# Optimization experiments

Measured on AMD Instinct MI355X. Metric: run time of the kernel, lower is better.

The kernel has to match this reference:

```python
import jax, jax.numpy as jnp
import numpy as np

N_NODES = 50000
N_EDGES = 800000
IN_CH = 128
OUT_CH = 32
HID = 2 * OUT_CH  # 64


def gcn_layer(x, W, b, src, dst, n):
    """PyG GCNConv: x' = D^-1/2 (A + I) D^-1/2 (x W) + b, flow source->target."""
    h = x @ W  # [n, out]
    # degree on target nodes, +1 for self loop
    deg = jax.ops.segment_sum(jnp.ones(dst.shape[0], h.dtype), dst, num_segments=n) + 1.0
    dis = jax.lax.rsqrt(deg)  # deg^-1/2
    norm = dis[src] * dis[dst]  # [E]
    msg = h[src] * norm[:, None]  # gather + scale, [E, out]
    agg = jax.ops.segment_sum(msg, dst, num_segments=n)  # scatter-add
    # self-loop contribution has norm dis[i]*dis[i] = 1/deg[i]
    return agg + h * (dis * dis)[:, None] + b


def setup_inputs() -> dict:
    key = jax.random.key(0)
    k1, k2, k3, k4, k5, k6 = jax.random.split(key, 6)
    x = jax.random.normal(k1, (N_NODES, IN_CH), dtype=jnp.float32)
    edge_index = jax.random.randint(k2, (2, N_EDGES), 0, N_NODES, dtype=jnp.int64)
    # Glorot-style init for GCN weights
    W1 = jax.random.normal(k3, (IN_CH, HID), dtype=jnp.float32) / np.sqrt(IN_CH)
    b1 = jnp.zeros((HID,), dtype=jnp.float32)
    W2 = jax.random.normal(k4, (HID, OUT_CH), dtype=jnp.float32) / np.sqrt(HID)
    b2 = jnp.zeros((OUT_CH,), dtype=jnp.float32)
    return {"x": x, "W1": W1, "b1": b1, "W2": W2, "b2": b2, "edge_index": edge_index}


def reference(x, W1, b1, W2, b2, edge_index):
    src, dst = edge_index[0], edge_index[1]
    h = jax.nn.relu(gcn_layer(x, W1, b1, src, dst, N_NODES))
    out = gcn_layer(h, W2, b2, src, dst, N_NODES)
    return out
```

## Files before the change

kernel.cpp:

```cpp
#include <hip/hip_runtime.h>
#include <hip/hip_bf16.h>
#include <cstddef>
#include <cstdint>

#define N_NODES 50000
#define N_EDGES 800000
#define IN_CH 128
#define HID 64
#define OUT_CH 32

#define NBUCK 196
#define BCAP2 5120
#define NBLK 256
#define EPB 3125
#define NT1 782

typedef __attribute__((ext_vector_type(8))) short bf16x8;
typedef __attribute__((ext_vector_type(8))) unsigned short u16x8;
typedef __attribute__((ext_vector_type(4))) float f32x4;

__device__ __forceinline__ unsigned short bf16rne(float f) {
    union { float f; unsigned u; } c; c.f = f;
    unsigned r = c.u + 0x7FFF + ((c.u >> 16) & 1);
    return (unsigned short)(r >> 16);
}
__device__ __forceinline__ float bf16f(unsigned short b) {
    union { unsigned u; float f; } c; c.u = ((unsigned)b) << 16;
    return c.f;
}

__device__ __forceinline__ void load_edge(const void* ei, int flag, int e, int& s, int& d) {
    if (flag) {
        const long long* p = (const long long*)ei;
        s = (int)p[e];
        d = (int)p[e + N_EDGES];
    } else {
        const int* p = (const int*)ei;
        s = p[e];
        d = p[e + N_EDGES];
    }
}

__global__ __launch_bounds__(256) void zerocur_kernel(int* __restrict__ cursor) {
    if (threadIdx.x < NBUCK) cursor[threadIdx.x] = 0;
}

__global__ __launch_bounds__(256) void scatter1_kernel(const void* ei,
                                                       int* __restrict__ cursor,
                                                       unsigned* __restrict__ packed) {
    __shared__ unsigned cbuf[EPB];
    __shared__ int h[NBUCK];
    __shared__ int lcur[NBUCK];
    __shared__ unsigned red[256];
    const int t = threadIdx.x;
    const int base = blockIdx.x * EPB;

    {
        unsigned acc = 0;
        const unsigned* w = (const unsigned*)ei;
        for (int i = t; i < 2048; i += 256) acc |= w[2 * i + 1];
        red[t] = acc;
    }
    if (t < NBUCK) h[t] = 0;
    __syncthreads();
    if (t < 128) red[t] |= red[t + 128];
    __syncthreads();
    if (t < 64) red[t] |= red[t + 64];
    __syncthreads();
    if (t == 0) {
        unsigned q = 0;
        for (int i = 0; i < 64; ++i) q |= red[i];
        red[0] = q;
    }
    __syncthreads();
    const int flag = (red[0] == 0) ? 1 : 0;

    for (int i = t; i < EPB; i += 256) {
        int s, d;
        load_edge(ei, flag, base + i, s, d);
        cbuf[i] = (unsigned)s | ((unsigned)d << 16);
        atomicAdd(&h[d >> 8], 1);
    }
    __syncthreads();
    if (t < NBUCK) lcur[t] = h[t] ? (t * BCAP2 + atomicAdd(&cursor[t], h[t])) : 0;
    __syncthreads();
    for (int i = t; i < EPB; i += 256) {
        unsigned p = cbuf[i];
        int b = p >> 24;
        int pos = atomicAdd(&lcur[b], 1);
        packed[pos] = p;
    }
}

__global__ __launch_bounds__(256) void buckgemm1_kernel(
        const int* __restrict__ cursor, unsigned* __restrict__ packed,
        unsigned* __restrict__ rowinfo, float* __restrict__ dis,
        const float* __restrict__ x, const float* __restrict__ W1,
        unsigned short* __restrict__ h1b) {
    __shared__ union {
        struct { int cnt[256]; int pref[256]; int lbuf[BCAP2]; } bk;
        struct { unsigned short xa[64][136]; unsigned short wb[64][136]; } g1;
    } u;
    const int t = threadIdx.x;

    if (blockIdx.x < NBUCK) {
        const int b = blockIdx.x;
        const int nodebase = b << 8;
        const int rbase = b * BCAP2;
        const int bsize = cursor[b];
        const int nb = min(256, N_NODES - nodebase);

        u.bk.cnt[t] = 0;
        __syncthreads();
        for (int i = t; i < bsize; i += 256)
            atomicAdd(&u.bk.cnt[(packed[rbase + i] >> 16) & 255], 1);
        __syncthreads();
        const int deg = u.bk.cnt[t];
        u.bk.pref[t] = deg;
        __syncthreads();
        for (int off = 1; off < 256; off <<= 1) {
            int q = (t >= off) ? u.bk.pref[t - off] : 0;
            __syncthreads();
            u.bk.pref[t] += q;
            __syncthreads();
        }
        const int excl = u.bk.pref[t] - deg;
        if (t < nb) {
            rowinfo[nodebase + t] = (unsigned)(rbase + excl) | ((unsigned)deg << 20);
            dis[nodebase + t] = rsqrtf((float)deg + 1.0f);
        }
        __syncthreads();
        u.bk.cnt[t] = excl;
        __syncthreads();
        for (int i = t; i < bsize; i += 256) {
            unsigned p = packed[rbase + i];
            int pos = atomicAdd(&u.bk.cnt[(p >> 16) & 255], 1);
            u.bk.lbuf[pos] = (int)(p & 0xFFFFu);
        }
        __syncthreads();
        for (int i = t; i < bsize; i += 256)
            packed[rbase + i] = (unsigned)u.bk.lbuf[i];
    } else {
        const int w = t >> 6;
        const int l = t & 63;
        const int brow = (blockIdx.x - NBUCK) * 64;

        for (int f = t; f < 64 * 32; f += 256) {
            int r = f >> 5, c = (f & 31) << 2;
            int gr = brow + r;
            float4 v = (gr < N_NODES) ? *(const float4*)(x + gr * IN_CH + c)
                                      : make_float4(0.f, 0.f, 0.f, 0.f);
            u.g1.xa[r][c + 0] = bf16rne(v.x); u.g1.xa[r][c + 1] = bf16rne(v.y);
            u.g1.xa[r][c + 2] = bf16rne(v.z); u.g1.xa[r][c + 3] = bf16rne(v.w);
        }
        for (int f = t; f < 128 * 16; f += 256) {
            int k = f >> 4, n = (f & 15) << 2;
            float4 v = *(const float4*)(W1 + k * HID + n);
            u.g1.wb[n + 0][k] = bf16rne(v.x); u.g1.wb[n + 1][k] = bf16rne(v.y);
            u.g1.wb[n + 2][k] = bf16rne(v.z); u.g1.wb[n + 3][k] = bf16rne(v.w);
        }
        __syncthreads();

        const int fr = l & 15;
        const int fk = (l >> 4) << 3;
        f32x4 acc[4] = {{0.f,0.f,0.f,0.f},{0.f,0.f,0.f,0.f},
                        {0.f,0.f,0.f,0.f},{0.f,0.f,0.f,0.f}};
#pragma unroll
        for (int kb = 0; kb < 4; ++kb) {
            const int k = kb * 32 + fk;
            bf16x8 a = *(const bf16x8*)&u.g1.xa[w * 16 + fr][k];
#pragma unroll
            for (int n = 0; n < 4; ++n) {
                bf16x8 bfr = *(const bf16x8*)&u.g1.wb[n * 16 + fr][k];
                acc[n] = __builtin_amdgcn_mfma_f32_16x16x32_bf16(a, bfr, acc[n], 0, 0, 0);
            }
        }
        const int rb = brow + w * 16 + ((l >> 4) << 2);
#pragma unroll
        for (int n = 0; n < 4; ++n) {
#pragma unroll
            for (int i = 0; i < 4; ++i) {
                int r = rb + i;
                if (r < N_NODES) h1b[r * HID + n * 16 + fr] = bf16rne(acc[n][i]);
            }
        }
    }
}

__global__ __launch_bounds__(256) void agg1_kernel(
        const unsigned* __restrict__ rowinfo, const unsigned* __restrict__ sorted,
        const float* __restrict__ dis, const unsigned short* __restrict__ h1b,
        const float* __restrict__ b1, unsigned short* __restrict__ agg1b) {
    const int l = threadIdx.x & 63;
    const int g = l >> 3;
    const int cl = l & 7;
    const int d = blockIdx.x * 4 + (threadIdx.x >> 6);
    if (d >= N_NODES) return;
    const unsigned ri = rowinfo[d];
    const int beg = (int)(ri & 0xFFFFFu);
    const int end = beg + (int)(ri >> 20);
    const float dd = dis[d];
    float a0 = 0.f, a1 = 0.f, a2 = 0.f, a3 = 0.f;
    float a4 = 0.f, a5 = 0.f, a6 = 0.f, a7 = 0.f;
    for (int j = beg + g; j < end; j += 8) {
        int s = (int)sorted[j];
        float n = dis[s] * dd;
        bf16x8 h = *(const bf16x8*)(h1b + s * HID + 8 * cl);
        a0 += bf16f((unsigned short)h[0]) * n; a1 += bf16f((unsigned short)h[1]) * n;
        a2 += bf16f((unsigned short)h[2]) * n; a3 += bf16f((unsigned short)h[3]) * n;
        a4 += bf16f((unsigned short)h[4]) * n; a5 += bf16f((unsigned short)h[5]) * n;
        a6 += bf16f((unsigned short)h[6]) * n; a7 += bf16f((unsigned short)h[7]) * n;
    }
#pragma unroll
    for (int st = 8; st <= 32; st <<= 1) {
        a0 += __shfl_xor(a0, st, 64); a1 += __shfl_xor(a1, st, 64);
        a2 += __shfl_xor(a2, st, 64); a3 += __shfl_xor(a3, st, 64);
        a4 += __shfl_xor(a4, st, 64); a5 += __shfl_xor(a5, st, 64);
        a6 += __shfl_xor(a6, st, 64); a7 += __shfl_xor(a7, st, 64);
    }
    if (g == 0) {
        bf16x8 hs = *(const bf16x8*)(h1b + d * HID + 8 * cl);
        float4 bv0 = *(const float4*)(b1 + 8 * cl);
        float4 bv1 = *(const float4*)(b1 + 8 * cl + 4);
        float d2 = dd * dd;
        u16x8 o;
        o[0] = bf16rne(fmaxf(a0 + bf16f((unsigned short)hs[0]) * d2 + bv0.x, 0.f));
        o[1] = bf16rne(fmaxf(a1 + bf16f((unsigned short)hs[1]) * d2 + bv0.y, 0.f));
        o[2] = bf16rne(fmaxf(a2 + bf16f((unsigned short)hs[2]) * d2 + bv0.z, 0.f));
        o[3] = bf16rne(fmaxf(a3 + bf16f((unsigned short)hs[3]) * d2 + bv0.w, 0.f));
        o[4] = bf16rne(fmaxf(a4 + bf16f((unsigned short)hs[4]) * d2 + bv1.x, 0.f));
        o[5] = bf16rne(fmaxf(a5 + bf16f((unsigned short)hs[5]) * d2 + bv1.y, 0.f));
        o[6] = bf16rne(fmaxf(a6 + bf16f((unsigned short)hs[6]) * d2 + bv1.z, 0.f));
        o[7] = bf16rne(fmaxf(a7 + bf16f((unsigned short)hs[7]) * d2 + bv1.w, 0.f));
        *(u16x8*)(agg1b + d * HID + 8 * cl) = o;
    }
}

__global__ __launch_bounds__(256) void gemm2_kernel(
        const unsigned short* __restrict__ agg1b, const float* __restrict__ W2,
        unsigned short* __restrict__ h2b) {
    __shared__ unsigned short xa[64][72];
    __shared__ unsigned short wb[32][72];
    const int t = threadIdx.x;
    const int w = t >> 6;
    const int l = t & 63;
    const int brow = blockIdx.x * 64;

    for (int f = t; f < 64 * 16; f += 256) {
        int r = f >> 4, c = (f & 15) << 2;
        int gr = brow + r;
        ushort4 v = make_ushort4(0, 0, 0, 0);
        if (gr < N_NODES) v = *(const ushort4*)(agg1b + gr * HID + c);
        *(ushort4*)&xa[r][c] = v;
    }
    for (int f = t; f < 64 * 8; f += 256) {
        int k = f >> 3, n = (f & 7) << 2;
        float4 v = *(const float4*)(W2 + k * OUT_CH + n);
        wb[n + 0][k] = bf16rne(v.x); wb[n + 1][k] = bf16rne(v.y);
        wb[n + 2][k] = bf16rne(v.z); wb[n + 3][k] = bf16rne(v.w);
    }
    __syncthreads();

    const int fr = l & 15;
    const int fk = (l >> 4) << 3;
    f32x4 acc[2] = {{0.f,0.f,0.f,0.f},{0.f,0.f,0.f,0.f}};
#pragma unroll
    for (int kb = 0; kb < 2; ++kb) {
        const int k = kb * 32 + fk;
        bf16x8 a = *(const bf16x8*)&xa[w * 16 + fr][k];
#pragma unroll
        for (int n = 0; n < 2; ++n) {
            bf16x8 bfr = *(const bf16x8*)&wb[n * 16 + fr][k];
            acc[n] = __builtin_amdgcn_mfma_f32_16x16x32_bf16(a, bfr, acc[n], 0, 0, 0);
        }
    }
    const int rb = brow + w * 16 + ((l >> 4) << 2);
#pragma unroll
    for (int n = 0; n < 2; ++n) {
#pragma unroll
        for (int i = 0; i < 4; ++i) {
            int r = rb + i;
            if (r < N_NODES) h2b[r * OUT_CH + n * 16 + fr] = bf16rne(acc[n][i]);
        }
    }
}

__global__ __launch_bounds__(256) void agg2_kernel(
        const unsigned* __restrict__ rowinfo, const unsigned* __restrict__ sorted,
        const float* __restrict__ dis, const unsigned short* __restrict__ h2b,
        const float* __restrict__ b2, float* __restrict__ out) {
    const int l = threadIdx.x & 63;
    const int g = l >> 2;
    const int cl = l & 3;
    const int d = blockIdx.x * 4 + (threadIdx.x >> 6);
    if (d >= N_NODES) return;
    const unsigned ri = rowinfo[d];
    const int beg = (int)(ri & 0xFFFFFu);
    const int end = beg + (int)(ri >> 20);
    const float dd = dis[d];
    float a0 = 0.f, a1 = 0.f, a2 = 0.f, a3 = 0.f;
    float a4 = 0.f, a5 = 0.f, a6 = 0.f, a7 = 0.f;
    for (int j = beg + g; j < end; j += 16) {
        int s = (int)sorted[j];
        float n = dis[s] * dd;
        bf16x8 h = *(const bf16x8*)(h2b + s * OUT_CH + 8 * cl);
        a0 += bf16f((unsigned short)h[0]) * n; a1 += bf16f((unsigned short)h[1]) * n;
        a2 += bf16f((unsigned short)h[2]) * n; a3 += bf16f((unsigned short)h[3]) * n;
        a4 += bf16f((unsigned short)h[4]) * n; a5 += bf16f((unsigned short)h[5]) * n;
        a6 += bf16f((unsigned short)h[6]) * n; a7 += bf16f((unsigned short)h[7]) * n;
    }
#pragma unroll
    for (int st = 4; st <= 32; st <<= 1) {
        a0 += __shfl_xor(a0, st, 64); a1 += __shfl_xor(a1, st, 64);
        a2 += __shfl_xor(a2, st, 64); a3 += __shfl_xor(a3, st, 64);
        a4 += __shfl_xor(a4, st, 64); a5 += __shfl_xor(a5, st, 64);
        a6 += __shfl_xor(a6, st, 64); a7 += __shfl_xor(a7, st, 64);
    }
    if (g == 0) {
        bf16x8 hs = *(const bf16x8*)(h2b + d * OUT_CH + 8 * cl);
        float4 bv0 = *(const float4*)(b2 + 8 * cl);
        float4 bv1 = *(const float4*)(b2 + 8 * cl + 4);
        float d2 = dd * dd;
        float4 o0, o1;
        o0.x = a0 + bf16f((unsigned short)hs[0]) * d2 + bv0.x;
        o0.y = a1 + bf16f((unsigned short)hs[1]) * d2 + bv0.y;
        o0.z = a2 + bf16f((unsigned short)hs[2]) * d2 + bv0.z;
        o0.w = a3 + bf16f((unsigned short)hs[3]) * d2 + bv0.w;
        o1.x = a4 + bf16f((unsigned short)hs[4]) * d2 + bv1.x;
        o1.y = a5 + bf16f((unsigned short)hs[5]) * d2 + bv1.y;
        o1.z = a6 + bf16f((unsigned short)hs[6]) * d2 + bv1.z;
        o1.w = a7 + bf16f((unsigned short)hs[7]) * d2 + bv1.w;
        *(float4*)(out + d * OUT_CH + 8 * cl) = o0;
        *(float4*)(out + d * OUT_CH + 8 * cl + 4) = o1;
    }
}

extern "C" void kernel_launch(void* const* d_in, const int* in_sizes, int n_in,
                              void* d_out, int out_size, void* d_ws, size_t ws_size,
                              hipStream_t stream) {
    const float* x  = (const float*)d_in[0];
    const float* W1 = (const float*)d_in[1];
    const float* b1 = (const float*)d_in[2];
    const float* W2 = (const float*)d_in[3];
    const float* b2 = (const float*)d_in[4];
    const void*  ei = d_in[5];
    float* out = (float*)d_out;

    char* wp = (char*)d_ws;
    auto alloc = [&](size_t n) { char* p = wp; wp += (n + 511) & ~(size_t)511; return p; };
    int*   cursor  = (int*)alloc(NBUCK * 4);
    unsigned* rowinfo = (unsigned*)alloc((size_t)N_NODES * 4);
    float* dis     = (float*)alloc((size_t)N_NODES * 4);
    unsigned* packed = (unsigned*)alloc((size_t)NBUCK * BCAP2 * 4);
    unsigned short* h1b = (unsigned short*)alloc((size_t)N_NODES * HID * 2);
    unsigned short* agg1b = (unsigned short*)alloc((size_t)N_NODES * HID * 2);
    unsigned short* h2b = (unsigned short*)alloc((size_t)N_NODES * OUT_CH * 2);

    zerocur_kernel<<<1, 256, 0, stream>>>(cursor);
    scatter1_kernel<<<NBLK, 256, 0, stream>>>(ei, cursor, packed);
    buckgemm1_kernel<<<NBUCK + NT1, 256, 0, stream>>>(cursor, packed, rowinfo, dis,
                                                      x, W1, h1b);
    agg1_kernel<<<(N_NODES + 3) / 4, 256, 0, stream>>>(rowinfo, packed, dis, h1b, b1, agg1b);
    gemm2_kernel<<<(N_NODES + 63) / 64, 256, 0, stream>>>(agg1b, W2, h2b);
    agg2_kernel<<<(N_NODES + 3) / 4, 256, 0, stream>>>(rowinfo, packed, dis, h2b, b2, out);
}
```

Measured before the change: 90.81 us.

## Fuse layer-1 aggregation with layer-2 GEMM through shared memory

Merges agg1 and gemm2 into one 1024-thread kernel. Each block aggregates 64 destination rows (16 waves, 4 rows each) into LDS, then 8 waves run MFMA against W2 to write h2b. This removes the agg1b intermediate round trip through global memory and one kernel launch. In exchange, blocks are much larger with a sync between phases, so waves that finish aggregation early sit idle and occupancy may drop.

```diff
diff --git a/kernel.cpp b/kernel.cpp
--- a/kernel.cpp
+++ b/kernel.cpp
@@ -187,100 +187,95 @@
     }
 }
 
-__global__ __launch_bounds__(256) void agg1_kernel(
+__global__ __launch_bounds__(1024) void agg1gemm2_kernel(
         const unsigned* __restrict__ rowinfo, const unsigned* __restrict__ sorted,
         const float* __restrict__ dis, const unsigned short* __restrict__ h1b,
-        const float* __restrict__ b1, unsigned short* __restrict__ agg1b) {
-    const int l = threadIdx.x & 63;
-    const int g = l >> 3;
-    const int cl = l & 7;
-    const int d = blockIdx.x * 4 + (threadIdx.x >> 6);
-    if (d >= N_NODES) return;
-    const unsigned ri = rowinfo[d];
-    const int beg = (int)(ri & 0xFFFFFu);
-    const int end = beg + (int)(ri >> 20);
-    const float dd = dis[d];
-    float a0 = 0.f, a1 = 0.f, a2 = 0.f, a3 = 0.f;
-    float a4 = 0.f, a5 = 0.f, a6 = 0.f, a7 = 0.f;
-    for (int j = beg + g; j < end; j += 8) {
-        int s = (int)sorted[j];
-        float n = dis[s] * dd;
-        bf16x8 h = *(const bf16x8*)(h1b + s * HID + 8 * cl);
-        a0 += bf16f((unsigned short)h[0]) * n; a1 += bf16f((unsigned short)h[1]) * n;
-        a2 += bf16f((unsigned short)h[2]) * n; a3 += bf16f((unsigned short)h[3]) * n;
-        a4 += bf16f((unsigned short)h[4]) * n; a5 += bf16f((unsigned short)h[5]) * n;
-        a6 += bf16f((unsigned short)h[6]) * n; a7 += bf16f((unsigned short)h[7]) * n;
-    }
-#pragma unroll
-    for (int st = 8; st <= 32; st <<= 1) {
-        a0 += __shfl_xor(a0, st, 64); a1 += __shfl_xor(a1, st, 64);
-        a2 += __shfl_xor(a2, st, 64); a3 += __shfl_xor(a3, st, 64);
-        a4 += __shfl_xor(a4, st, 64); a5 += __shfl_xor(a5, st, 64);
-        a6 += __shfl_xor(a6, st, 64); a7 += __shfl_xor(a7, st, 64);
-    }
-    if (g == 0) {
-        bf16x8 hs = *(const bf16x8*)(h1b + d * HID + 8 * cl);
-        float4 bv0 = *(const float4*)(b1 + 8 * cl);
-        float4 bv1 = *(const float4*)(b1 + 8 * cl + 4);
-        float d2 = dd * dd;
-        u16x8 o;
-        o[0] = bf16rne(fmaxf(a0 + bf16f((unsigned short)hs[0]) * d2 + bv0.x, 0.f));
-        o[1] = bf16rne(fmaxf(a1 + bf16f((unsigned short)hs[1]) * d2 + bv0.y, 0.f));
-        o[2] = bf16rne(fmaxf(a2 + bf16f((unsigned short)hs[2]) * d2 + bv0.z, 0.f));
-        o[3] = bf16rne(fmaxf(a3 + bf16f((unsigned short)hs[3]) * d2 + bv0.w, 0.f));
-        o[4] = bf16rne(fmaxf(a4 + bf16f((unsigned short)hs[4]) * d2 + bv1.x, 0.f));
-        o[5] = bf16rne(fmaxf(a5 + bf16f((unsigned short)hs[5]) * d2 + bv1.y, 0.f));
-        o[6] = bf16rne(fmaxf(a6 + bf16f((unsigned short)hs[6]) * d2 + bv1.z, 0.f));
-        o[7] = bf16rne(fmaxf(a7 + bf16f((unsigned short)hs[7]) * d2 + bv1.w, 0.f));
-        *(u16x8*)(agg1b + d * HID + 8 * cl) = o;
-    }
-}
-
-__global__ __launch_bounds__(256) void gemm2_kernel(
-        const unsigned short* __restrict__ agg1b, const float* __restrict__ W2,
+        const float* __restrict__ b1, const float* __restrict__ W2,
         unsigned short* __restrict__ h2b) {
     __shared__ unsigned short xa[64][72];
     __shared__ unsigned short wb[32][72];
     const int t = threadIdx.x;
     const int w = t >> 6;
     const int l = t & 63;
-    const int brow = blockIdx.x * 64;
-
-    for (int f = t; f < 64 * 16; f += 256) {
-        int r = f >> 4, c = (f & 15) << 2;
-        int gr = brow + r;
-        ushort4 v = make_ushort4(0, 0, 0, 0);
-        if (gr < N_NODES) v = *(const ushort4*)(agg1b + gr * HID + c);
-        *(ushort4*)&xa[r][c] = v;
-    }
-    for (int f = t; f < 64 * 8; f += 256) {
-        int k = f >> 3, n = (f & 7) << 2;
+    const int g = l >> 3;
+    const int cl = l & 7;
+    const int base = blockIdx.x * 64;
+
+    if (t < 512) {
+        int k = t >> 3, n = (t & 7) << 2;
         float4 v = *(const float4*)(W2 + k * OUT_CH + n);
         wb[n + 0][k] = bf16rne(v.x); wb[n + 1][k] = bf16rne(v.y);
         wb[n + 2][k] = bf16rne(v.z); wb[n + 3][k] = bf16rne(v.w);
     }
-    __syncthreads();
-
-    const int fr = l & 15;
-    const int fk = (l >> 4) << 3;
-    f32x4 acc[2] = {{0.f,0.f,0.f,0.f},{0.f,0.f,0.f,0.f}};
-#pragma unroll
-    for (int kb = 0; kb < 2; ++kb) {
-        const int k = kb * 32 + fk;
-        bf16x8 a = *(const bf16x8*)&xa[w * 16 + fr][k];
-#pragma unroll
-        for (int n = 0; n < 2; ++n) {
-            bf16x8 bfr = *(const bf16x8*)&wb[n * 16 + fr][k];
-            acc[n] = __builtin_amdgcn_mfma_f32_16x16x32_bf16(a, bfr, acc[n], 0, 0, 0);
-        }
-    }
-    const int rb = brow + w * 16 + ((l >> 4) << 2);
-#pragma unroll
-    for (int n = 0; n < 2; ++n) {
+
+#pragma unroll
+    for (int q = 0; q < 4; ++q) {
+        const int row = w * 4 + q;
+        const int d = base + row;
+        float a0 = 0.f, a1 = 0.f, a2 = 0.f, a3 = 0.f;
+        float a4 = 0.f, a5 = 0.f, a6 = 0.f, a7 = 0.f;
+        if (d < N_NODES) {
+            const unsigned ri = rowinfo[d];
+            const int beg = (int)(ri & 0xFFFFFu);
+            const int end = beg + (int)(ri >> 20);
+            const float dd = dis[d];
+            for (int j = beg + g; j < end; j += 8) {
+                int s = (int)sorted[j];
+                float n = dis[s] * dd;
+                bf16x8 h = *(const bf16x8*)(h1b + s * HID + 8 * cl);
+                a0 += bf16f((unsigned short)h[0]) * n; a1 += bf16f((unsigned short)h[1]) * n;
+                a2 += bf16f((unsigned short)h[2]) * n; a3 += bf16f((unsigned short)h[3]) * n;
+                a4 += bf16f((unsigned short)h[4]) * n; a5 += bf16f((unsigned short)h[5]) * n;
+                a6 += bf16f((unsigned short)h[6]) * n; a7 += bf16f((unsigned short)h[7]) * n;
+            }
+#pragma unroll
+            for (int st = 8; st <= 32; st <<= 1) {
+                a0 += __shfl_xor(a0, st, 64); a1 += __shfl_xor(a1, st, 64);
+                a2 += __shfl_xor(a2, st, 64); a3 += __shfl_xor(a3, st, 64);
+                a4 += __shfl_xor(a4, st, 64); a5 += __shfl_xor(a5, st, 64);
+                a6 += __shfl_xor(a6, st, 64); a7 += __shfl_xor(a7, st, 64);
+            }
+            if (g == 0) {
+                bf16x8 hs = *(const bf16x8*)(h1b + d * HID + 8 * cl);
+                float4 bv0 = *(const float4*)(b1 + 8 * cl);
+                float4 bv1 = *(const float4*)(b1 + 8 * cl + 4);
+                const float dd2 = dd * dd;
+                u16x8 o;
+                o[0] = bf16rne(fmaxf(a0 + bf16f((unsigned short)hs[0]) * dd2 + bv0.x, 0.f));
+                o[1] = bf16rne(fmaxf(a1 + bf16f((unsigned short)hs[1]) * dd2 + bv0.y, 0.f));
+                o[2] = bf16rne(fmaxf(a2 + bf16f((unsigned short)hs[2]) * dd2 + bv0.z, 0.f));
+                o[3] = bf16rne(fmaxf(a3 + bf16f((unsigned short)hs[3]) * dd2 + bv0.w, 0.f));
+                o[4] = bf16rne(fmaxf(a4 + bf16f((unsigned short)hs[4]) * dd2 + bv1.x, 0.f));
+                o[5] = bf16rne(fmaxf(a5 + bf16f((unsigned short)hs[5]) * dd2 + bv1.y, 0.f));
+                o[6] = bf16rne(fmaxf(a6 + bf16f((unsigned short)hs[6]) * dd2 + bv1.z, 0.f));
+                o[7] = bf16rne(fmaxf(a7 + bf16f((unsigned short)hs[7]) * dd2 + bv1.w, 0.f));
+                *(u16x8*)&xa[row][8 * cl] = o;
+            }
+        } else if (g == 0) {
+            u16x8 z = {0, 0, 0, 0, 0, 0, 0, 0};
+            *(u16x8*)&xa[row][8 * cl] = z;
+        }
+    }
+    __syncthreads();
+
+    if (w < 8) {
+        const int rt = (w >> 1) << 4;
+        const int ct = (w & 1) << 4;
+        const int fr = l & 15;
+        const int fk = (l >> 4) << 3;
+        f32x4 acc = {0.f, 0.f, 0.f, 0.f};
+#pragma unroll
+        for (int kb = 0; kb < 2; ++kb) {
+            const int k = kb * 32 + fk;
+            bf16x8 a = *(const bf16x8*)&xa[rt + fr][k];
+            bf16x8 bfr = *(const bf16x8*)&wb[ct + fr][k];
+            acc = __builtin_amdgcn_mfma_f32_16x16x32_bf16(a, bfr, acc, 0, 0, 0);
+        }
+        const int rb = base + rt + ((l >> 4) << 2);
 #pragma unroll
         for (int i = 0; i < 4; ++i) {
             int r = rb + i;
-            if (r < N_NODES) h2b[r * OUT_CH + n * 16 + fr] = bf16rne(acc[n][i]);
+            if (r < N_NODES) h2b[r * OUT_CH + ct + fr] = bf16rne(acc[i]);
         }
     }
 }
@@ -353,14 +348,12 @@
     float* dis     = (float*)alloc((size_t)N_NODES * 4);
     unsigned* packed = (unsigned*)alloc((size_t)NBUCK * BCAP2 * 4);
     unsigned short* h1b = (unsigned short*)alloc((size_t)N_NODES * HID * 2);
-    unsigned short* agg1b = (unsigned short*)alloc((size_t)N_NODES * HID * 2);
     unsigned short* h2b = (unsigned short*)alloc((size_t)N_NODES * OUT_CH * 2);
 
     zerocur_kernel<<<1, 256, 0, stream>>>(cursor);
     scatter1_kernel<<<NBLK, 256, 0, stream>>>(ei, cursor, packed);
     buckgemm1_kernel<<<NBUCK + NT1, 256, 0, stream>>>(cursor, packed, rowinfo, dis,
                                                       x, W1, h1b);
-    agg1_kernel<<<(N_NODES + 3) / 4, 256, 0, stream>>>(rowinfo, packed, dis, h1b, b1, agg1b);
-    gemm2_kernel<<<(N_NODES + 63) / 64, 256, 0, stream>>>(agg1b, W2, h2b);
+    agg1gemm2_kernel<<<NT1, 1024, 0, stream>>>(rowinfo, packed, dis, h1b, b1, W2, h2b);
     agg2_kernel<<<(N_NODES + 3) / 4, 256, 0, stream>>>(rowinfo, packed, dis, h2b, b2, out);
 }
```

Result: no change. 91.51 us (+0.8%).
